# Kernel tuning notes

Measured on AMD Instinct MI355X. Metric: run time of the kernel, lower is better.

The kernel has to match this reference:

```python
import jax, jax.numpy as jnp
import numpy as np

# Fixed problem sizes (uniform frames so the irregular loop vectorizes)
S = 32            # number of frames (sequences)
N = 128           # pedestrians per frame
H = 64            # pool_h_dim (lstm hidden dim)
G = 8             # grid_size
NS = 2.0          # neighbourhood_size
OUT = 64          # pool_out_dim
EPS = 1e-5        # BatchNorm1d eps


def setup_inputs() -> dict:
    key = jax.random.key(0)
    k1, k2, k3 = jax.random.split(key, 3)
    hidden_states = jax.random.normal(k1, (S * N, H), jnp.float32)
    # positions in [0, 4): neighbourhood of size 2 captures many neighbours
    all_pos = jax.random.uniform(k2, (S * N, 2), jnp.float32) * 4.0
    W = jax.random.normal(k3, (G * G * H, OUT), jnp.float32) * 0.02
    b = jnp.zeros((OUT,), jnp.float32)
    gamma = jnp.ones((OUT,), jnp.float32)
    beta = jnp.zeros((OUT,), jnp.float32)
    starts = jnp.arange(S, dtype=jnp.int32) * N
    seq_start_end = jnp.stack([starts, starts + N], axis=1)
    return {"hidden_states": hidden_states, "all_pos": all_pos, "W": W,
            "b": b, "gamma": gamma, "beta": beta,
            "seq_start_end": seq_start_end}


def _pool_one_frame(hs, ps):
    # hs: [N, H] hidden states, ps: [N, 2] positions of one frame.
    # Pair (i, j): bbox around ped i, contribution from ped j's hidden state.
    xi, yi = ps[:, 0][:, None], ps[:, 1][:, None]   # bbox owner i -> rows
    xj, yj = ps[:, 0][None, :], ps[:, 1][None, :]   # neighbour j -> cols
    half = NS / 2
    tlx, tly = xi - half, yi + half                 # top-left of bbox(i)
    brx, bry = xi + half, yi - half                 # bottom-right of bbox(i)
    gx = jnp.floor((xj - tlx) / NS * G)
    gy = jnp.floor((tly - yj) / NS * G)
    grid = (gx + G * gy).astype(jnp.int32) + 1      # +1: slot 0 is dump bin
    # out-of-bbox or self -> masked to bin 0
    mask = ((xj <= tlx) | (yj >= tly) | (xj >= brx) | (yj <= bry)
            | jnp.eye(N, dtype=bool))
    grid = grid + (jnp.arange(N, dtype=jnp.int32) * (G * G))[:, None]
    grid = jnp.where(mask, 0, grid)                 # [N, N]
    vals = jnp.broadcast_to(hs[None, :, :], (N, N, H)).reshape(N * N, H)
    pooled = jax.ops.segment_sum(vals, grid.reshape(-1),
                                 num_segments=N * G * G + 1)[1:]
    return pooled.reshape(N, G * G * H)


def reference(hidden_states, all_pos, W, b, gamma, beta, seq_start_end):
    h = hidden_states.reshape(S, N, H)
    p = all_pos.reshape(S, N, 2)
    pool_h = jax.vmap(_pool_one_frame)(h, p).reshape(S * N, G * G * H)
    x = pool_h @ W + b
    # BatchNorm1d in training mode: biased batch statistics
    mean = jnp.mean(x, axis=0)
    var = jnp.mean((x - mean) ** 2, axis=0)
    x = (x - mean) / jnp.sqrt(var + EPS) * gamma + beta
    return jax.nn.relu(x)
```

## Files before the change

kernel.cpp:

```cpp
#include <hip/hip_runtime.h>
#include <math.h>

#define NFRAMES 32
#define NPED    128
#define HDIM    64
#define KDIM    4096
#define OUTD    64
#define EPSV    1e-5f
#define NBLK    256
#define PROW    4104
#define HROW    136

typedef __attribute__((ext_vector_type(8))) short  short8;
typedef __attribute__((ext_vector_type(4))) float  floatx4;

static __device__ __forceinline__ unsigned short f2bf(float f) {
    union { float f; unsigned u; } v; v.f = f;
    unsigned r = v.u + 0x7fffu + ((v.u >> 16) & 1u);
    return (unsigned short)(r >> 16);
}

static __device__ __forceinline__ int kperm(int k) {
    return (k & 0xC0F) | ((k >> 2) & 0x0F0) | ((k & 0x030) << 4);
}

__global__ void k_wt(const float* __restrict__ W, unsigned short* __restrict__ Wt) {
    __shared__ float T[64 * 65];
    const int t  = threadIdx.x;
    const int k0 = blockIdx.x * 64;
    #pragma unroll
    for (int it = 0; it < 16; ++it) {
        int idx = it * 256 + t;
        int kl = idx >> 6, o = idx & 63;
        T[kl * 65 + o] = W[(size_t)(k0 + kl) * OUTD + o];
    }
    __syncthreads();
    {
        int o   = t & 63;
        int seg = t >> 6;
        int kl  = seg * 16;
        unsigned pk[8];
        #pragma unroll
        for (int e = 0; e < 8; ++e) {
            pk[e] = (unsigned)f2bf(T[(kl + 2 * e) * 65 + o]) |
                    ((unsigned)f2bf(T[(kl + 2 * e + 1) * 65 + o]) << 16);
        }
        unsigned short* dst = Wt + (size_t)o * KDIM + kperm(k0 + kl);
        ((uint4*)dst)[0] = (uint4){pk[0], pk[1], pk[2], pk[3]};
        ((uint4*)dst)[1] = (uint4){pk[4], pk[5], pk[6], pk[7]};
    }
}

__global__ __launch_bounds__(512, 2) void k_fused(
    const float* __restrict__ hs, const float* __restrict__ pos,
    const unsigned short* __restrict__ Wt,
    float* __restrict__ x, float* __restrict__ psumT, float* __restrict__ psumsqT)
{
    __shared__ unsigned short P[16 * PROW];
    __shared__ unsigned short HsT[HDIM * HROW];
    __shared__ unsigned char  CT[16 * NPED];
    __shared__ float posL[NPED * 2];

    const int tid   = threadIdx.x;
    const int bid   = blockIdx.x;
    const int f     = bid >> 3;
    const int chunk = bid & 7;
    const int lane  = tid & 63;
    const int w     = tid >> 6;
    const int m     = lane & 15;
    const int quad  = lane >> 4;

    if (tid < 256) posL[tid] = pos[f * (NPED * 2) + tid];
    const float* hsF = hs + f * (NPED * HDIM);
    #pragma unroll
    for (int it = 0; it < 4; ++it) {
        int g = it * 512 + tid;
        float4 v = ((const float4*)hsF)[g];
        int j  = g >> 4;
        int h0 = (g & 15) * 4;
        HsT[(h0 + 0) * HROW + j] = f2bf(v.x);
        HsT[(h0 + 1) * HROW + j] = f2bf(v.y);
        HsT[(h0 + 2) * HROW + j] = f2bf(v.z);
        HsT[(h0 + 3) * HROW + j] = f2bf(v.w);
    }
    __syncthreads();

    const int i0 = chunk * 16;
    #pragma unroll
    for (int it = 0; it < 4; ++it) {
        int idx = it * 512 + tid;
        int i = idx >> 7, j = idx & 127;
        float xi = posL[(i0 + i) * 2], yi = posL[(i0 + i) * 2 + 1];
        float xj = posL[j * 2],        yj = posL[j * 2 + 1];
        float tlx = xi - 1.0f, tly = yi + 1.0f;
        bool valid = (xj > tlx) & (yj < tly) & (xj < xi + 1.0f) &
                     (yj > yi - 1.0f) & (j != i0 + i);
        int gx = (int)floorf((xj - tlx) * 4.0f);
        int gy = (int)floorf((tly - yj) * 4.0f);
        int c  = gx + 8 * gy;
        CT[i * NPED + j] = (valid && (unsigned)c < 64u) ? (unsigned char)c : 255;
    }

    short8 Af[4][4];
    #pragma unroll
    for (int ht = 0; ht < 4; ++ht)
        #pragma unroll
        for (int kt = 0; kt < 4; ++kt)
            Af[ht][kt] = *(const short8*)&HsT[(ht * 16 + m) * HROW + kt * 32 + quad * 8];
    __syncthreads();

    #pragma unroll
    for (int r = 0; r < 2; ++r) {
        const int i = w * 2 + r;
        const unsigned char* ctRow = CT + i * NPED;
        floatx4 pa[4][4];
        #pragma unroll
        for (int ht = 0; ht < 4; ++ht)
            #pragma unroll
            for (int ct = 0; ct < 4; ++ct) pa[ht][ct] = (floatx4){0.f, 0.f, 0.f, 0.f};
        #pragma unroll
        for (int kt = 0; kt < 4; ++kt) {
            unsigned long long cb = *(const unsigned long long*)(ctRow + kt * 32 + quad * 8);
            unsigned lo = (unsigned)cb, hi = (unsigned)(cb >> 32);
            int b0 = (int)(lo & 255u), b1 = (int)((lo >> 8) & 255u);
            int b2 = (int)((lo >> 16) & 255u), b3 = (int)(lo >> 24);
            int b4 = (int)(hi & 255u), b5 = (int)((hi >> 8) & 255u);
            int b6 = (int)((hi >> 16) & 255u), b7 = (int)(hi >> 24);
            #pragma unroll
            for (int ct = 0; ct < 4; ++ct) {
                const int tgt = ct * 16 + m;
                union { int iv[4]; short8 sv; } B;
                B.iv[0] = (b0 == tgt ? 0x00003F80 : 0) | (b1 == tgt ? 0x3F800000 : 0);
                B.iv[1] = (b2 == tgt ? 0x00003F80 : 0) | (b3 == tgt ? 0x3F800000 : 0);
                B.iv[2] = (b4 == tgt ? 0x00003F80 : 0) | (b5 == tgt ? 0x3F800000 : 0);
                B.iv[3] = (b6 == tgt ? 0x00003F80 : 0) | (b7 == tgt ? 0x3F800000 : 0);
                #pragma unroll
                for (int ht = 0; ht < 4; ++ht)
                    pa[ht][ct] = __builtin_amdgcn_mfma_f32_16x16x32_bf16(Af[ht][kt], B.sv, pa[ht][ct], 0, 0, 0);
            }
        }
        #pragma unroll
        for (int ct = 0; ct < 4; ++ct)
            #pragma unroll
            for (int ht = 0; ht < 4; ++ht) {
                union { floatx4 fv; unsigned uv[4]; } U; U.fv = pa[ht][ct];
                uint2 pv;
                pv.x = __builtin_amdgcn_perm(U.uv[1], U.uv[0], 0x07060302u);
                pv.y = __builtin_amdgcn_perm(U.uv[3], U.uv[2], 0x07060302u);
                *reinterpret_cast<uint2*>(&P[i * PROW + ct * 1024 + ht * 256 + m * 16 + quad * 4]) = pv;
            }
    }
    __syncthreads();

    const int wn = w & 3;
    const int wh = w >> 2;
    floatx4 acc[4];
    #pragma unroll
    for (int u = 0; u < 4; ++u) acc[u] = (floatx4){0.f, 0.f, 0.f, 0.f};
    const unsigned short* Prow  = P + m * PROW + wh * 2048;
    const unsigned short* WtRow = Wt + (size_t)(wn * 16 + m) * KDIM + wh * 2048;
    #pragma unroll 4
    for (int kk = 0; kk < 2048; kk += 128) {
        #pragma unroll
        for (int u = 0; u < 4; ++u) {
            int k0 = kk + u * 32 + quad * 8;
            short8 a = *(const short8*)(Prow + k0);
            short8 b = *(const short8*)(WtRow + k0);
            acc[u] = __builtin_amdgcn_mfma_f32_16x16x32_bf16(a, b, acc[u], 0, 0, 0);
        }
    }
    floatx4 accf = (acc[0] + acc[1]) + (acc[2] + acc[3]);

    float* red = (float*)HsT;
    if (wh == 1) *(floatx4*)(red + (wn * 64 + lane) * 4) = accf;
    __syncthreads();

    if (wh == 0) {
        accf += *(const floatx4*)(red + (wn * 64 + lane) * 4);
        const int ibase = f * NPED + chunk * 16;
        float s1 = 0.f, s2 = 0.f;
        #pragma unroll
        for (int r = 0; r < 4; ++r) {
            float v = accf[r];
            int row = quad * 4 + r;
            x[(size_t)(ibase + row) * OUTD + wn * 16 + m] = v;
            s1 += v; s2 += v * v;
        }
        s1 += __shfl_xor(s1, 16); s1 += __shfl_xor(s1, 32);
        s2 += __shfl_xor(s2, 16); s2 += __shfl_xor(s2, 32);
        if (lane < 16) {
            psumT  [(wn * 16 + lane) * NBLK + bid] = s1;
            psumsqT[(wn * 16 + lane) * NBLK + bid] = s2;
        }
    }
}

__global__ __launch_bounds__(512) void k_apply(
    const float* __restrict__ x, const float* __restrict__ psumT,
    const float* __restrict__ psumsqT, const float* __restrict__ gamma,
    const float* __restrict__ beta, float* __restrict__ out) {
    __shared__ float muL[OUTD], isL[OUTD];
    const int t = threadIdx.x;
    const int o = t >> 3, p = t & 7;
    float s1 = 0.f, s2 = 0.f;
    const float4* q1 = (const float4*)(psumT   + o * NBLK + p * 32);
    const float4* q2 = (const float4*)(psumsqT + o * NBLK + p * 32);
    #pragma unroll
    for (int i = 0; i < 8; ++i) {
        float4 a = q1[i], b = q2[i];
        s1 += (a.x + a.y) + (a.z + a.w);
        s2 += (b.x + b.y) + (b.z + b.w);
    }
    #pragma unroll
    for (int d = 1; d < 8; d <<= 1) {
        s1 += __shfl_xor(s1, d);
        s2 += __shfl_xor(s2, d);
    }
    if (p == 0) {
        const float inv_n = 1.0f / (float)(NFRAMES * NPED);
        float mu  = s1 * inv_n;
        float var = s2 * inv_n - mu * mu;
        muL[o] = mu;
        isL[o] = rsqrtf(var + EPSV);
    }
    __syncthreads();
    #pragma unroll
    for (int i = 0; i < 4; ++i) {
        int g  = blockIdx.x * 2048 + i * 512 + t;
        int o0 = (g & 15) * 4;
        float4 xv = ((const float4*)x)[g];
        float4 r;
        r.x = (xv.x - muL[o0 + 0]) * isL[o0 + 0] * gamma[o0 + 0] + beta[o0 + 0];
        r.y = (xv.y - muL[o0 + 1]) * isL[o0 + 1] * gamma[o0 + 1] + beta[o0 + 1];
        r.z = (xv.z - muL[o0 + 2]) * isL[o0 + 2] * gamma[o0 + 2] + beta[o0 + 2];
        r.w = (xv.w - muL[o0 + 3]) * isL[o0 + 3] * gamma[o0 + 3] + beta[o0 + 3];
        r.x = r.x > 0.f ? r.x : 0.f;
        r.y = r.y > 0.f ? r.y : 0.f;
        r.z = r.z > 0.f ? r.z : 0.f;
        r.w = r.w > 0.f ? r.w : 0.f;
        ((float4*)out)[g] = r;
    }
}

extern "C" void kernel_launch(void* const* d_in, const int* in_sizes, int n_in,
                              void* d_out, int out_size, void* d_ws, size_t ws_size,
                              hipStream_t stream) {
    const float* hs    = (const float*)d_in[0];
    const float* pos   = (const float*)d_in[1];
    const float* W     = (const float*)d_in[2];
    const float* gamma = (const float*)d_in[4];
    const float* beta  = (const float*)d_in[5];

    char* ws = (char*)d_ws;
    unsigned short* Wt = (unsigned short*)ws;
    float* x       = (float*)(ws + (512 << 10));
    float* psumT   = (float*)(ws + (512 << 10) + (1 << 20));
    float* psumsqT = psumT + NBLK * OUTD;

    k_wt   <<<KDIM / 64, 256, 0, stream>>>(W, Wt);
    k_fused<<<NBLK, 512, 0, stream>>>(hs, pos, Wt, x, psumT, psumsqT);
    k_apply<<<32, 512, 0, stream>>>(x, psumT, psumsqT, gamma, beta, (float*)d_out);
}
```

Baseline: 96.73 us.

## Halve rows per block, alias shared memory, and pre-swizzle W for coalesced MFMA loads

Each fused block now handles 8 pedestrians instead of 16, doubling the grid to 512 blocks. Shared memory is aliased (P over HsT and the reduction buffer) so the launch bound can request 4 blocks per CU. The weight transpose kernel now writes W in a per-lane fragment layout so each wave's B loads in the GEMM are contiguous 16-byte vectors. The trade-off is that half of the MFMA M dimension is wasted on duplicated rows, the psum buffers are larger, and an extra barrier is added before the reduction.

```diff
diff --git a/kernel.cpp b/kernel.cpp
--- a/kernel.cpp
+++ b/kernel.cpp
@@ -7,8 +7,9 @@
 #define KDIM    4096
 #define OUTD    64
 #define EPSV    1e-5f
-#define NBLK    256
-#define PROW    4104
+#define NBLK    512
+#define MROW    8
+#define PROW    4112
 #define HROW    136
 
 typedef __attribute__((ext_vector_type(8))) short  short8;
@@ -29,42 +30,48 @@
     const int t  = threadIdx.x;
     const int k0 = blockIdx.x * 64;
     #pragma unroll
-    for (int it = 0; it < 16; ++it) {
-        int idx = it * 256 + t;
+    for (int it = 0; it < 8; ++it) {
+        int idx = it * 512 + t;
         int kl = idx >> 6, o = idx & 63;
         T[kl * 65 + o] = W[(size_t)(k0 + kl) * OUTD + o];
     }
     __syncthreads();
     {
-        int o   = t & 63;
-        int seg = t >> 6;
-        int kl  = seg * 16;
-        unsigned pk[8];
+        int o  = t & 63;
+        int kl = (t >> 6) * 8;
+        unsigned pk[4];
         #pragma unroll
-        for (int e = 0; e < 8; ++e) {
+        for (int e = 0; e < 4; ++e) {
             pk[e] = (unsigned)f2bf(T[(kl + 2 * e) * 65 + o]) |
                     ((unsigned)f2bf(T[(kl + 2 * e + 1) * 65 + o]) << 16);
         }
-        unsigned short* dst = Wt + (size_t)o * KDIM + kperm(k0 + kl);
-        ((uint4*)dst)[0] = (uint4){pk[0], pk[1], pk[2], pk[3]};
-        ((uint4*)dst)[1] = (uint4){pk[4], pk[5], pk[6], pk[7]};
-    }
-}
-
-__global__ __launch_bounds__(512, 2) void k_fused(
+        int klog = kperm(k0 + kl);
+        int wn   = o >> 4;
+        int wq   = klog >> 11;
+        int s    = (klog >> 5) & 63;
+        int quad = (klog >> 3) & 3;
+        int ln   = quad * 16 + (o & 15);
+        unsigned short* dst = Wt + ((size_t)((wn * 2 + wq) * 64 + s) * 64 + ln) * 8;
+        *(uint4*)dst = (uint4){pk[0], pk[1], pk[2], pk[3]};
+    }
+}
+
+__global__ __launch_bounds__(512, 4) void k_fused(
     const float* __restrict__ hs, const float* __restrict__ pos,
     const unsigned short* __restrict__ Wt,
     float* __restrict__ x, float* __restrict__ psumT, float* __restrict__ psumsqT)
 {
-    __shared__ unsigned short P[16 * PROW];
-    __shared__ unsigned short HsT[HDIM * HROW];
-    __shared__ unsigned char  CT[16 * NPED];
-    __shared__ float posL[NPED * 2];
+    __shared__ char SM[MROW * PROW * 2 + 1024 + 1024];
+    unsigned short* P    = (unsigned short*)SM;
+    unsigned short* HsT  = (unsigned short*)SM;
+    float*          red  = (float*)SM;
+    unsigned char*  CT   = (unsigned char*)(SM + MROW * PROW * 2);
+    float*          posL = (float*)(SM + MROW * PROW * 2 + 1024);
 
     const int tid   = threadIdx.x;
     const int bid   = blockIdx.x;
-    const int f     = bid >> 3;
-    const int chunk = bid & 7;
+    const int f     = bid >> 4;
+    const int chunk = bid & 15;
     const int lane  = tid & 63;
     const int w     = tid >> 6;
     const int m     = lane & 15;
@@ -85,9 +92,9 @@
     }
     __syncthreads();
 
-    const int i0 = chunk * 16;
-    #pragma unroll
-    for (int it = 0; it < 4; ++it) {
+    const int i0 = chunk * 8;
+    #pragma unroll
+    for (int it = 0; it < 2; ++it) {
         int idx = it * 512 + tid;
         int i = idx >> 7, j = idx & 127;
         float xi = posL[(i0 + i) * 2], yi = posL[(i0 + i) * 2 + 1];
@@ -109,82 +116,81 @@
             Af[ht][kt] = *(const short8*)&HsT[(ht * 16 + m) * HROW + kt * 32 + quad * 8];
     __syncthreads();
 
-    #pragma unroll
-    for (int r = 0; r < 2; ++r) {
-        const int i = w * 2 + r;
-        const unsigned char* ctRow = CT + i * NPED;
-        floatx4 pa[4][4];
+    {
+        const unsigned char* ctRow = CT + w * NPED;
         #pragma unroll
-        for (int ht = 0; ht < 4; ++ht)
-            #pragma unroll
-            for (int ct = 0; ct < 4; ++ct) pa[ht][ct] = (floatx4){0.f, 0.f, 0.f, 0.f};
-        #pragma unroll
-        for (int kt = 0; kt < 4; ++kt) {
-            unsigned long long cb = *(const unsigned long long*)(ctRow + kt * 32 + quad * 8);
-            unsigned lo = (unsigned)cb, hi = (unsigned)(cb >> 32);
-            int b0 = (int)(lo & 255u), b1 = (int)((lo >> 8) & 255u);
-            int b2 = (int)((lo >> 16) & 255u), b3 = (int)(lo >> 24);
-            int b4 = (int)(hi & 255u), b5 = (int)((hi >> 8) & 255u);
-            int b6 = (int)((hi >> 16) & 255u), b7 = (int)(hi >> 24);
-            #pragma unroll
-            for (int ct = 0; ct < 4; ++ct) {
-                const int tgt = ct * 16 + m;
-                union { int iv[4]; short8 sv; } B;
-                B.iv[0] = (b0 == tgt ? 0x00003F80 : 0) | (b1 == tgt ? 0x3F800000 : 0);
-                B.iv[1] = (b2 == tgt ? 0x00003F80 : 0) | (b3 == tgt ? 0x3F800000 : 0);
-                B.iv[2] = (b4 == tgt ? 0x00003F80 : 0) | (b5 == tgt ? 0x3F800000 : 0);
-                B.iv[3] = (b6 == tgt ? 0x00003F80 : 0) | (b7 == tgt ? 0x3F800000 : 0);
+        for (int ch = 0; ch < 2; ++ch) {
+            floatx4 pa[4][2];
+            #pragma unroll
+            for (int ht = 0; ht < 4; ++ht)
                 #pragma unroll
-                for (int ht = 0; ht < 4; ++ht)
-                    pa[ht][ct] = __builtin_amdgcn_mfma_f32_16x16x32_bf16(Af[ht][kt], B.sv, pa[ht][ct], 0, 0, 0);
+                for (int c2 = 0; c2 < 2; ++c2) pa[ht][c2] = (floatx4){0.f, 0.f, 0.f, 0.f};
+            #pragma unroll
+            for (int kt = 0; kt < 4; ++kt) {
+                unsigned long long cb = *(const unsigned long long*)(ctRow + kt * 32 + quad * 8);
+                unsigned lo = (unsigned)cb, hi = (unsigned)(cb >> 32);
+                int b0 = (int)(lo & 255u), b1 = (int)((lo >> 8) & 255u);
+                int b2 = (int)((lo >> 16) & 255u), b3 = (int)(lo >> 24);
+                int b4 = (int)(hi & 255u), b5 = (int)((hi >> 8) & 255u);
+                int b6 = (int)((hi >> 16) & 255u), b7 = (int)(hi >> 24);
+                #pragma unroll
+                for (int c2 = 0; c2 < 2; ++c2) {
+                    const int tgt = (ch * 2 + c2) * 16 + m;
+                    union { int iv[4]; short8 sv; } B;
+                    B.iv[0] = (b0 == tgt ? 0x00003F80 : 0) | (b1 == tgt ? 0x3F800000 : 0);
+                    B.iv[1] = (b2 == tgt ? 0x00003F80 : 0) | (b3 == tgt ? 0x3F800000 : 0);
+                    B.iv[2] = (b4 == tgt ? 0x00003F80 : 0) | (b5 == tgt ? 0x3F800000 : 0);
+                    B.iv[3] = (b6 == tgt ? 0x00003F80 : 0) | (b7 == tgt ? 0x3F800000 : 0);
+                    #pragma unroll
+                    for (int ht = 0; ht < 4; ++ht)
+                        pa[ht][c2] = __builtin_amdgcn_mfma_f32_16x16x32_bf16(Af[ht][kt], B.sv, pa[ht][c2], 0, 0, 0);
+                }
             }
-        }
-        #pragma unroll
-        for (int ct = 0; ct < 4; ++ct)
-            #pragma unroll
-            for (int ht = 0; ht < 4; ++ht) {
-                union { floatx4 fv; unsigned uv[4]; } U; U.fv = pa[ht][ct];
-                uint2 pv;
-                pv.x = __builtin_amdgcn_perm(U.uv[1], U.uv[0], 0x07060302u);
-                pv.y = __builtin_amdgcn_perm(U.uv[3], U.uv[2], 0x07060302u);
-                *reinterpret_cast<uint2*>(&P[i * PROW + ct * 1024 + ht * 256 + m * 16 + quad * 4]) = pv;
+            #pragma unroll
+            for (int c2 = 0; c2 < 2; ++c2)
+                #pragma unroll
+                for (int ht = 0; ht < 4; ++ht) {
+                    union { floatx4 fv; unsigned uv[4]; } U; U.fv = pa[ht][c2];
+                    uint2 pv;
+                    pv.x = __builtin_amdgcn_perm(U.uv[1], U.uv[0], 0x07060302u);
+                    pv.y = __builtin_amdgcn_perm(U.uv[3], U.uv[2], 0x07060302u);
+                    *reinterpret_cast<uint2*>(&P[w * PROW + (ch * 2 + c2) * 1024 + ht * 256 + m * 16 + quad * 4]) = pv;
+                }
+        }
+    }
+    __syncthreads();
+
+    const int wn = w & 3;
+    const int wq = w >> 2;
+    floatx4 acc[4];
+    #pragma unroll
+    for (int u = 0; u < 4; ++u) acc[u] = (floatx4){0.f, 0.f, 0.f, 0.f};
+    const unsigned short* Prow = P + (m & 7) * PROW + wq * 2048;
+    const unsigned short* wB   = Wt + ((size_t)(wn * 2 + wq) * 64 * 64 + lane) * 8;
+    #pragma unroll 8
+    for (int s = 0; s < 64; ++s) {
+        short8 a = *(const short8*)(Prow + s * 32 + quad * 8);
+        short8 b = *(const short8*)(wB + s * 512);
+        acc[s & 3] = __builtin_amdgcn_mfma_f32_16x16x32_bf16(a, b, acc[s & 3], 0, 0, 0);
+    }
+    floatx4 accf = (acc[0] + acc[1]) + (acc[2] + acc[3]);
+    __syncthreads();
+
+    if (wq == 1) *(floatx4*)(red + (wn * 64 + lane) * 4) = accf;
+    __syncthreads();
+
+    if (wq == 0) {
+        accf += *(const floatx4*)(red + (wn * 64 + lane) * 4);
+        const int ibase = f * NPED + chunk * 8;
+        float s1 = 0.f, s2 = 0.f;
+        if (quad < 2) {
+            #pragma unroll
+            for (int r = 0; r < 4; ++r) {
+                float v = accf[r];
+                int row = quad * 4 + r;
+                x[(size_t)(ibase + row) * OUTD + wn * 16 + m] = v;
+                s1 += v; s2 += v * v;
             }
-    }
-    __syncthreads();
-
-    const int wn = w & 3;
-    const int wh = w >> 2;
-    floatx4 acc[4];
-    #pragma unroll
-    for (int u = 0; u < 4; ++u) acc[u] = (floatx4){0.f, 0.f, 0.f, 0.f};
-    const unsigned short* Prow  = P + m * PROW + wh * 2048;
-    const unsigned short* WtRow = Wt + (size_t)(wn * 16 + m) * KDIM + wh * 2048;
-    #pragma unroll 4
-    for (int kk = 0; kk < 2048; kk += 128) {
-        #pragma unroll
-        for (int u = 0; u < 4; ++u) {
-            int k0 = kk + u * 32 + quad * 8;
-            short8 a = *(const short8*)(Prow + k0);
-            short8 b = *(const short8*)(WtRow + k0);
-            acc[u] = __builtin_amdgcn_mfma_f32_16x16x32_bf16(a, b, acc[u], 0, 0, 0);
-        }
-    }
-    floatx4 accf = (acc[0] + acc[1]) + (acc[2] + acc[3]);
-
-    float* red = (float*)HsT;
-    if (wh == 1) *(floatx4*)(red + (wn * 64 + lane) * 4) = accf;
-    __syncthreads();
-
-    if (wh == 0) {
-        accf += *(const floatx4*)(red + (wn * 64 + lane) * 4);
-        const int ibase = f * NPED + chunk * 16;
-        float s1 = 0.f, s2 = 0.f;
-        #pragma unroll
-        for (int r = 0; r < 4; ++r) {
-            float v = accf[r];
-            int row = quad * 4 + r;
-            x[(size_t)(ibase + row) * OUTD + wn * 16 + m] = v;
-            s1 += v; s2 += v * v;
         }
         s1 += __shfl_xor(s1, 16); s1 += __shfl_xor(s1, 32);
         s2 += __shfl_xor(s2, 16); s2 += __shfl_xor(s2, 32);
@@ -203,10 +209,10 @@
     const int t = threadIdx.x;
     const int o = t >> 3, p = t & 7;
     float s1 = 0.f, s2 = 0.f;
-    const float4* q1 = (const float4*)(psumT   + o * NBLK + p * 32);
-    const float4* q2 = (const float4*)(psumsqT + o * NBLK + p * 32);
-    #pragma unroll
-    for (int i = 0; i < 8; ++i) {
+    const float4* q1 = (const float4*)(psumT   + o * NBLK + p * 64);
+    const float4* q2 = (const float4*)(psumsqT + o * NBLK + p * 64);
+    #pragma unroll
+    for (int i = 0; i < 16; ++i) {
         float4 a = q1[i], b = q2[i];
         s1 += (a.x + a.y) + (a.z + a.w);
         s2 += (b.x + b.y) + (b.z + b.w);
@@ -257,7 +263,7 @@
     float* psumT   = (float*)(ws + (512 << 10) + (1 << 20));
     float* psumsqT = psumT + NBLK * OUTD;
 
-    k_wt   <<<KDIM / 64, 256, 0, stream>>>(W, Wt);
+    k_wt   <<<KDIM / 64, 512, 0, stream>>>(W, Wt);
     k_fused<<<NBLK, 512, 0, stream>>>(hs, pos, Wt, x, psumT, psumsqT);
     k_apply<<<32, 512, 0, stream>>>(x, psumT, psumsqT, gamma, beta, (float*)d_out);
 }
```

New measurement: 93.22 us, median of 2. 1.04x faster.
